# Kernel tuning notes

Hardware: AMD Instinct MI355X
Metric: run time of the kernel (lower is better)

The kernel has to match this reference:

```python
import jax, jax.numpy as jnp
import numpy as np

EPS = 1e-10  # matches torch float32 path


def setup_inputs() -> dict:
    key = jax.random.key(0)
    ks = jax.random.split(key, 8)
    B, E, D, N = 32, 32000, 128, 1000
    scale = 1.0 / np.sqrt(D)
    return {
        "edge_attr": jax.random.normal(ks[0], (B, E, D), dtype=jnp.float32),
        "edge_index": jax.random.randint(ks[1], (B, 2, E), 0, N, dtype=jnp.int64),
        "W1": jax.random.normal(ks[2], (D, D), dtype=jnp.float32) * scale,
        "b1": jax.random.normal(ks[3], (D,), dtype=jnp.float32) * 0.01,
        "W2": jax.random.normal(ks[4], (D, D), dtype=jnp.float32) * scale,
        "b2": jax.random.normal(ks[5], (D,), dtype=jnp.float32) * 0.01,
        "Wout": jax.random.normal(ks[6], (1, D), dtype=jnp.float32) * scale,
        "bout": jax.random.normal(ks[7], (1,), dtype=jnp.float32) * 0.01,
        "num_nodes": N,
    }


def reference(edge_attr, edge_index, W1, b1, W2, b2, Wout, bout, num_nodes):
    # Edge MLP: (num_layers-1)=2 hidden silu linears, then 1-dim sigmoid output
    x = jax.nn.silu(jnp.einsum("bed,fd->bef", edge_attr, W1) + b1)
    x = jax.nn.silu(jnp.einsum("bed,fd->bef", x, W2) + b2)
    vals = jax.nn.sigmoid(jnp.einsum("bed,od->beo", x, Wout) + bout)[..., 0]  # [B, E]
    B = vals.shape[0]
    b_idx = jnp.arange(B)[:, None]  # [B, 1] broadcasts over E
    heatmap = jnp.zeros((B, num_nodes, num_nodes), dtype=vals.dtype)
    heatmap = heatmap.at[b_idx, edge_index[:, 0], edge_index[:, 1]].set(vals)
    return jnp.log(heatmap + EPS)
```

## Files before the change

### kernel.cpp

```cpp
#include <hip/hip_runtime.h>
#include <stdint.h>
#include <string.h>
#include <math.h>

typedef __bf16 bf16x8 __attribute__((ext_vector_type(8)));
typedef float f32x4 __attribute__((ext_vector_type(4)));
typedef unsigned short us8 __attribute__((ext_vector_type(8)));
typedef unsigned int u32;

#define DD 128

__device__ __forceinline__ unsigned short f2bf(float f) {
    __bf16 b = (__bf16)f;
    return __builtin_bit_cast(unsigned short, b);
}
__device__ __forceinline__ u32 pack2(float a, float b) {
    return (u32)f2bf(a) | ((u32)f2bf(b) << 16);
}
__device__ __forceinline__ float fsilu(float x) {
    float e = __expf(-x);
    return x * __builtin_amdgcn_rcpf(1.0f + e);
}

__device__ __forceinline__ float decz(u32 u) {
    float z = (float)(int)(u & 0x3FFFu) * (1.0f / 256.0f) - 40.0f;
    float s = __builtin_amdgcn_rcpf(1.0f + __expf(-z));
    return __logf(s + 1e-10f);
}
__global__ void decode_sparse(u32* __restrict__ p, long n4, u32 le) {
    long i  = (long)blockIdx.x * blockDim.x + threadIdx.x;
    long st = (long)gridDim.x * blockDim.x;
    for (long k = i; k < n4; k += st) {
        uint4 u = ((const uint4*)p)[k];
        float* f = (float*)(p + k * 4);
        if (u.x >= 0xE0000000u) f[0] = decz(u.x); else if (u.x != le) ((u32*)f)[0] = le;
        if (u.y >= 0xE0000000u) f[1] = decz(u.y); else if (u.y != le) ((u32*)f)[1] = le;
        if (u.z >= 0xE0000000u) f[2] = decz(u.z); else if (u.z != le) ((u32*)f)[2] = le;
        if (u.w >= 0xE0000000u) f[3] = decz(u.w); else if (u.w != le) ((u32*)f)[3] = le;
    }
}

__global__ __launch_bounds__(1024)
void mlp_scatter(const float* __restrict__ A,
                 const int* __restrict__ eidx,
                 const float* __restrict__ W1, const float* __restrict__ B1,
                 const float* __restrict__ W2, const float* __restrict__ B2,
                 const float* __restrict__ WO, const float* __restrict__ BO,
                 u32* __restrict__ out,
                 int E, int nWT, int N)
{
    extern __shared__ char smem[];
    unsigned short* W1s = (unsigned short*)smem;
    unsigned short* W2s = (unsigned short*)(smem + 32768);
    float* b1s = (float*)(smem + 65536);
    float* b2s = (float*)(smem + 66048);
    float* wos = (float*)(smem + 66560);
    char*  Hs  = smem + 67072;

    const int tid  = threadIdx.x;
    const int lane = tid & 63;
    const int wave = tid >> 6;
    const int lrow = lane & 15;
    const int lg   = lane >> 4;

    #pragma unroll
    for (int c = 0; c < 2; ++c) {
        int id = c * 1024 + tid;
        int f  = id >> 4;
        int kb = (id & 15) * 8;
        const float* s1 = W1 + f * DD + kb;
        const float* s2 = W2 + f * DD + kb;
        float4 a0 = *(const float4*)s1, a1 = *(const float4*)(s1 + 4);
        float4 c0 = *(const float4*)s2, c1 = *(const float4*)(s2 + 4);
        us8 t1, t2;
        t1[0]=f2bf(a0.x); t1[1]=f2bf(a0.y); t1[2]=f2bf(a0.z); t1[3]=f2bf(a0.w);
        t1[4]=f2bf(a1.x); t1[5]=f2bf(a1.y); t1[6]=f2bf(a1.z); t1[7]=f2bf(a1.w);
        t2[0]=f2bf(c0.x); t2[1]=f2bf(c0.y); t2[2]=f2bf(c0.z); t2[3]=f2bf(c0.w);
        t2[4]=f2bf(c1.x); t2[5]=f2bf(c1.y); t2[6]=f2bf(c1.z); t2[7]=f2bf(c1.w);
        int off = f * 256 + ((kb * 2) ^ ((f & 7) << 4));
        *(us8*)((char*)W1s + off) = t1;
        *(us8*)((char*)W2s + off) = t2;
    }
    if (tid < DD) { b1s[tid] = B1[tid]; b2s[tid] = B2[tid]; wos[tid] = WO[tid]; }
    const float bo = BO[0];
    const size_t NN = (size_t)N * (size_t)N;
    char* HsW = Hs + wave * 4096;
    __syncthreads();

    const int wid  = blockIdx.x * 16 + wave;
    const int step = (int)gridDim.x * 16;
    if (wid >= nWT) return;

    float4 va[8];
    {
        const float* Ar = A + (size_t)((wid << 4) + lrow) * DD;
        #pragma unroll
        for (int kk = 0; kk < 4; ++kk) {
            const float* p = Ar + kk * 32 + lg * 8;
            va[2 * kk]     = *(const float4*)p;
            va[2 * kk + 1] = *(const float4*)(p + 4);
        }
    }

    for (int wt = wid; wt < nWT; wt += step) {
        const int r0  = wt << 4;
        const int b   = r0 / E;
        const int ei0 = r0 - b * E;
        int i0 = 0, j0 = 0;
        if (lane < 16) {
            i0 = eidx[(size_t)(2 * b) * E + ei0 + lane];
            j0 = eidx[(size_t)(2 * b + 1) * E + ei0 + lane];
        }

        bf16x8 ef[4];
        #pragma unroll
        for (int kk = 0; kk < 4; ++kk) {
            us8 t;
            t[0]=f2bf(va[2*kk].x);   t[1]=f2bf(va[2*kk].y);
            t[2]=f2bf(va[2*kk].z);   t[3]=f2bf(va[2*kk].w);
            t[4]=f2bf(va[2*kk+1].x); t[5]=f2bf(va[2*kk+1].y);
            t[6]=f2bf(va[2*kk+1].z); t[7]=f2bf(va[2*kk+1].w);
            ef[kk] = __builtin_bit_cast(bf16x8, t);
        }

        {
            int tn = wt + step; if (tn >= nWT) tn = wt;
            const float* Ar = A + (size_t)((tn << 4) + lrow) * DD;
            #pragma unroll
            for (int kk = 0; kk < 4; ++kk) {
                const float* p = Ar + kk * 32 + lg * 8;
                va[2 * kk]     = *(const float4*)p;
                va[2 * kk + 1] = *(const float4*)(p + 4);
            }
        }

        f32x4 acc[8];
        #pragma unroll
        for (int mt = 0; mt < 8; ++mt)
            acc[mt] = *(const f32x4*)&b1s[mt * 16 + lg * 4];
        #pragma unroll
        for (int kk = 0; kk < 4; ++kk)
            #pragma unroll
            for (int mt = 0; mt < 8; ++mt) {
                int f = mt * 16 + lrow;
                bf16x8 wf = *(const bf16x8*)((const char*)W1s + f * 256 +
                                             ((kk * 64 + lg * 16) ^ ((f & 7) << 4)));
                acc[mt] = __builtin_amdgcn_mfma_f32_16x16x32_bf16(wf, ef[kk], acc[mt], 0, 0, 0);
            }

        #pragma unroll
        for (int mt = 0; mt < 8; ++mt) {
            u32 p0 = pack2(fsilu(acc[mt][0]), fsilu(acc[mt][1]));
            u32 p1 = pack2(fsilu(acc[mt][2]), fsilu(acc[mt][3]));
            *(uint2*)(HsW + lrow * 256 + ((mt * 32 + lg * 8) ^ ((lrow & 7) << 4))) =
                make_uint2(p0, p1);
        }

        f32x4 acc2[8];
        #pragma unroll
        for (int mt = 0; mt < 8; ++mt)
            acc2[mt] = *(const f32x4*)&b2s[mt * 16 + lg * 4];
        #pragma unroll
        for (int kk = 0; kk < 4; ++kk) {
            bf16x8 hf = *(const bf16x8*)(HsW + lrow * 256 +
                                         ((kk * 64 + lg * 16) ^ ((lrow & 7) << 4)));
            #pragma unroll
            for (int mt = 0; mt < 8; ++mt) {
                int f = mt * 16 + lrow;
                bf16x8 wf = *(const bf16x8*)((const char*)W2s + f * 256 +
                                             ((kk * 64 + lg * 16) ^ ((f & 7) << 4)));
                acc2[mt] = __builtin_amdgcn_mfma_f32_16x16x32_bf16(wf, hf, acc2[mt], 0, 0, 0);
            }
        }

        float zp = 0.f;
        #pragma unroll
        for (int mt = 0; mt < 8; ++mt) {
            f32x4 w4 = *(const f32x4*)&wos[mt * 16 + lg * 4];
            zp += w4[0] * fsilu(acc2[mt][0]) + w4[1] * fsilu(acc2[mt][1])
                + w4[2] * fsilu(acc2[mt][2]) + w4[3] * fsilu(acc2[mt][3]);
        }
        zp += __shfl_xor(zp, 16);
        zp += __shfl_xor(zp, 32);

        if (lane < 16) {
            float z = zp + bo;
            int qz = (int)((z + 40.0f) * 256.0f + 0.5f);
            qz = qz < 0 ? 0 : (qz > 16383 ? 16383 : qz);
            u32 packed = 0xE0000000u | ((u32)(ei0 + lane + 1) << 14) | (u32)qz;
            atomicMax(&out[(size_t)b * NN + (size_t)i0 * N + (size_t)j0], packed);
        }
    }
}

extern "C" void kernel_launch(void* const* d_in, const int* in_sizes, int n_in,
                              void* d_out, int out_size, void* d_ws, size_t ws_size,
                              hipStream_t stream) {
    const float* edge_attr  = (const float*)d_in[0];
    const int*   edge_index = (const int*)d_in[1];
    const float* W1   = (const float*)d_in[2];
    const float* b1   = (const float*)d_in[3];
    const float* W2   = (const float*)d_in[4];
    const float* b2   = (const float*)d_in[5];
    const float* Wout = (const float*)d_in[6];
    const float* bout = (const float*)d_in[7];

    long rows = (long)in_sizes[0] / DD;
    int  E    = in_sizes[1] / 64;
    int  nWT  = (int)(rows / 16);
    int  Bb   = (int)(rows / E);
    int  N    = (int)(sqrtf((float)(out_size / Bb)) + 0.5f);

    u32* outp = (u32*)d_out;
    long n4 = (long)out_size >> 2;

    float fv = logf(1e-10f);
    u32 LE; memcpy(&LE, &fv, 4);

    const int SMEM = 132608;
    hipFuncSetAttribute((const void*)mlp_scatter,
                        hipFuncAttributeMaxDynamicSharedMemorySize, SMEM);

    mlp_scatter<<<256, 1024, SMEM, stream>>>(edge_attr, edge_index, W1, b1, W2, b2,
                                             Wout, bout, outp, E, nWT, N);
    decode_sparse<<<2048, 256, 0, stream>>>(outp, n4, LE);
}
```

Measured before the change: 184.2 us.

## Switch MLP matmuls from bf16 to fp8 MFMA with fragment-ordered LDS layout

Weights, input activations and the hidden layer are converted to fp8 and fed to 16x16x32 fp8 MFMA instead of bf16. Weights and the hidden tile are stored in LDS in per-lane fragment order, so each lane reads one 8-byte word with no XOR swizzle. This halves LDS use and LDS read bytes and cheapens the conversions. The cost is much lower numerical precision in both hidden layers, which could push the log-sigmoid outputs past tolerance. The kernel is also dominated by HBM traffic for edge_attr and the heatmap, so the compute savings may not show up in total time.

```diff
diff --git a/kernel.cpp b/kernel.cpp
--- a/kernel.cpp
+++ b/kernel.cpp
@@ -3,23 +3,18 @@
 #include <string.h>
 #include <math.h>
 
-typedef __bf16 bf16x8 __attribute__((ext_vector_type(8)));
 typedef float f32x4 __attribute__((ext_vector_type(4)));
-typedef unsigned short us8 __attribute__((ext_vector_type(8)));
 typedef unsigned int u32;
 
 #define DD 128
 
-__device__ __forceinline__ unsigned short f2bf(float f) {
-    __bf16 b = (__bf16)f;
-    return __builtin_bit_cast(unsigned short, b);
-}
-__device__ __forceinline__ u32 pack2(float a, float b) {
-    return (u32)f2bf(a) | ((u32)f2bf(b) << 16);
-}
 __device__ __forceinline__ float fsilu(float x) {
     float e = __expf(-x);
     return x * __builtin_amdgcn_rcpf(1.0f + e);
+}
+__device__ __forceinline__ u32 pk4fp8(float a, float b, float c, float d) {
+    u32 r = __builtin_amdgcn_cvt_pk_fp8_f32(a, b, 0u, false);
+    return __builtin_amdgcn_cvt_pk_fp8_f32(c, d, r, true);
 }
 
 __device__ __forceinline__ float decz(u32 u) {
@@ -50,12 +45,12 @@
                  int E, int nWT, int N)
 {
     extern __shared__ char smem[];
-    unsigned short* W1s = (unsigned short*)smem;
-    unsigned short* W2s = (unsigned short*)(smem + 32768);
-    float* b1s = (float*)(smem + 65536);
-    float* b2s = (float*)(smem + 66048);
-    float* wos = (float*)(smem + 66560);
-    char*  Hs  = smem + 67072;
+    uint2* W1s = (uint2*)smem;
+    uint2* W2s = (uint2*)(smem + 16384);
+    float* b1s = (float*)(smem + 32768);
+    float* b2s = (float*)(smem + 33280);
+    float* wos = (float*)(smem + 33792);
+    uint2* Hs  = (uint2*)(smem + 34304);
 
     const int tid  = threadIdx.x;
     const int lane = tid & 63;
@@ -66,25 +61,20 @@
     #pragma unroll
     for (int c = 0; c < 2; ++c) {
         int id = c * 1024 + tid;
-        int f  = id >> 4;
-        int kb = (id & 15) * 8;
-        const float* s1 = W1 + f * DD + kb;
-        const float* s2 = W2 + f * DD + kb;
-        float4 a0 = *(const float4*)s1, a1 = *(const float4*)(s1 + 4);
-        float4 c0 = *(const float4*)s2, c1 = *(const float4*)(s2 + 4);
-        us8 t1, t2;
-        t1[0]=f2bf(a0.x); t1[1]=f2bf(a0.y); t1[2]=f2bf(a0.z); t1[3]=f2bf(a0.w);
-        t1[4]=f2bf(a1.x); t1[5]=f2bf(a1.y); t1[6]=f2bf(a1.z); t1[7]=f2bf(a1.w);
-        t2[0]=f2bf(c0.x); t2[1]=f2bf(c0.y); t2[2]=f2bf(c0.z); t2[3]=f2bf(c0.w);
-        t2[4]=f2bf(c1.x); t2[5]=f2bf(c1.y); t2[6]=f2bf(c1.z); t2[7]=f2bf(c1.w);
-        int off = f * 256 + ((kb * 2) ^ ((f & 7) << 4));
-        *(us8*)((char*)W1s + off) = t1;
-        *(us8*)((char*)W2s + off) = t2;
+        int mt = id >> 8, kk = (id >> 6) & 3, ln = id & 63;
+        const float* p1 = W1 + (mt * 16 + (ln & 15)) * DD + kk * 32 + (ln >> 4) * 8;
+        const float* p2 = W2 + (mt * 16 + (ln & 15)) * DD + kk * 32 + (ln >> 4) * 8;
+        float4 x0 = *(const float4*)p1, x1 = *(const float4*)(p1 + 4);
+        float4 y0 = *(const float4*)p2, y1 = *(const float4*)(p2 + 4);
+        W1s[mt * 256 + kk * 64 + ln] = make_uint2(pk4fp8(x0.x, x0.y, x0.z, x0.w),
+                                                  pk4fp8(x1.x, x1.y, x1.z, x1.w));
+        W2s[mt * 256 + kk * 64 + ln] = make_uint2(pk4fp8(y0.x, y0.y, y0.z, y0.w),
+                                                  pk4fp8(y1.x, y1.y, y1.z, y1.w));
     }
     if (tid < DD) { b1s[tid] = B1[tid]; b2s[tid] = B2[tid]; wos[tid] = WO[tid]; }
     const float bo = BO[0];
     const size_t NN = (size_t)N * (size_t)N;
-    char* HsW = Hs + wave * 4096;
+    uint2* HsW = Hs + wave * 256;
     __syncthreads();
 
     const int wid  = blockIdx.x * 16 + wave;
@@ -112,16 +102,12 @@
             j0 = eidx[(size_t)(2 * b + 1) * E + ei0 + lane];
         }
 
-        bf16x8 ef[4];
-        #pragma unroll
-        for (int kk = 0; kk < 4; ++kk) {
-            us8 t;
-            t[0]=f2bf(va[2*kk].x);   t[1]=f2bf(va[2*kk].y);
-            t[2]=f2bf(va[2*kk].z);   t[3]=f2bf(va[2*kk].w);
-            t[4]=f2bf(va[2*kk+1].x); t[5]=f2bf(va[2*kk+1].y);
-            t[6]=f2bf(va[2*kk+1].z); t[7]=f2bf(va[2*kk+1].w);
-            ef[kk] = __builtin_bit_cast(bf16x8, t);
-        }
+        uint2 ef[4];
+        #pragma unroll
+        for (int kk = 0; kk < 4; ++kk)
+            ef[kk] = make_uint2(
+                pk4fp8(va[2*kk].x,   va[2*kk].y,   va[2*kk].z,   va[2*kk].w),
+                pk4fp8(va[2*kk+1].x, va[2*kk+1].y, va[2*kk+1].z, va[2*kk+1].w));
 
         {
             int tn = wt + step; if (tn >= nWT) tn = wt;
@@ -141,19 +127,17 @@
         #pragma unroll
         for (int kk = 0; kk < 4; ++kk)
             #pragma unroll
-            for (int mt = 0; mt < 8; ++mt) {
-                int f = mt * 16 + lrow;
-                bf16x8 wf = *(const bf16x8*)((const char*)W1s + f * 256 +
-                                             ((kk * 64 + lg * 16) ^ ((f & 7) << 4)));
-                acc[mt] = __builtin_amdgcn_mfma_f32_16x16x32_bf16(wf, ef[kk], acc[mt], 0, 0, 0);
-            }
+            for (int mt = 0; mt < 8; ++mt)
+                acc[mt] = __builtin_amdgcn_mfma_f32_16x16x32_fp8_fp8(
+                    __builtin_bit_cast(long, W1s[mt * 256 + kk * 64 + lane]),
+                    __builtin_bit_cast(long, ef[kk]), acc[mt], 0, 0, 0);
 
         #pragma unroll
         for (int mt = 0; mt < 8; ++mt) {
-            u32 p0 = pack2(fsilu(acc[mt][0]), fsilu(acc[mt][1]));
-            u32 p1 = pack2(fsilu(acc[mt][2]), fsilu(acc[mt][3]));
-            *(uint2*)(HsW + lrow * 256 + ((mt * 32 + lg * 8) ^ ((lrow & 7) << 4))) =
-                make_uint2(p0, p1);
+            int lnp = (((mt & 1) << 1) | (lg >> 1)) * 16 + lrow;
+            u32 pw = pk4fp8(fsilu(acc[mt][0]), fsilu(acc[mt][1]),
+                            fsilu(acc[mt][2]), fsilu(acc[mt][3]));
+            ((u32*)&HsW[(mt >> 1) * 64 + lnp])[lg & 1] = pw;
         }
 
         f32x4 acc2[8];
@@ -162,15 +146,12 @@
             acc2[mt] = *(const f32x4*)&b2s[mt * 16 + lg * 4];
         #pragma unroll
         for (int kk = 0; kk < 4; ++kk) {
-            bf16x8 hf = *(const bf16x8*)(HsW + lrow * 256 +
-                                         ((kk * 64 + lg * 16) ^ ((lrow & 7) << 4)));
+            long hf = __builtin_bit_cast(long, HsW[kk * 64 + lane]);
             #pragma unroll
-            for (int mt = 0; mt < 8; ++mt) {
-                int f = mt * 16 + lrow;
-                bf16x8 wf = *(const bf16x8*)((const char*)W2s + f * 256 +
-                                             ((kk * 64 + lg * 16) ^ ((f & 7) << 4)));
-                acc2[mt] = __builtin_amdgcn_mfma_f32_16x16x32_bf16(wf, hf, acc2[mt], 0, 0, 0);
-            }
+            for (int mt = 0; mt < 8; ++mt)
+                acc2[mt] = __builtin_amdgcn_mfma_f32_16x16x32_fp8_fp8(
+                    __builtin_bit_cast(long, W2s[mt * 256 + kk * 64 + lane]),
+                    hf, acc2[mt], 0, 0, 0);
         }
 
         float zp = 0.f;
@@ -217,7 +198,7 @@
     float fv = logf(1e-10f);
     u32 LE; memcpy(&LE, &fv, 4);
 
-    const int SMEM = 132608;
+    const int SMEM = 67072;
     hipFuncSetAttribute((const void*)mlp_scatter,
                         hipFuncAttributeMaxDynamicSharedMemorySize, SMEM);
 
```

After: 179.7 us, median of 3. 2.5% less time.
